# Kernel tuning notes

Measured on AMD Instinct MI355X. Metric: run time of the kernel, lower is better.

The kernel has to match this reference:

```python
import jax, jax.numpy as jnp
import numpy as np

DIM = 64; N_C = 2000; N_P = 1500; N_ATOMS = 40; L_PROT = 512
N_FP = 10000; N_WORD = 8000; DIM_D = 1024; DIM_P = 1024
L_GNN = 3; L_CNN = 3; L_GCN = 2; WIN = 5; B = 4096


def setup_inputs() -> dict:
    key = jax.random.key(0)
    ks = jax.random.split(key, 32)
    g = lambda i, shape, s=0.05: jax.random.normal(ks[i], shape, dtype=jnp.float32) * s
    inp = {}
    inp["idx_c"] = jax.random.randint(ks[0], (B,), 0, N_C)
    inp["idx_p"] = jax.random.randint(ks[1], (B,), 0, N_P)
    inp["compounds"] = jax.random.randint(ks[2], (N_C, N_ATOMS), 0, N_FP)
    inp["proteins"] = jax.random.randint(ks[3], (N_P, L_PROT), 0, N_WORD)
    a = (jax.random.uniform(ks[4], (N_C, N_ATOMS, N_ATOMS)) < 0.1).astype(jnp.float32)
    inp["adjacencies"] = jnp.clip(a + jnp.swapaxes(a, 1, 2) + jnp.eye(N_ATOMS), 0.0, 1.0)
    ac = (jax.random.uniform(ks[5], (N_C, N_C)) < 0.005).astype(jnp.float32)
    inp["A_c"] = jnp.clip(ac + ac.T + jnp.eye(N_C), 0.0, 1.0) / 20.0
    ap = (jax.random.uniform(ks[6], (N_P, N_P)) < 0.005).astype(jnp.float32)
    inp["A_p"] = jnp.clip(ap + ap.T + jnp.eye(N_P), 0.0, 1.0) / 20.0
    inp["embed_fp"] = g(7, (N_FP, DIM), 1.0)
    inp["embed_word"] = g(8, (N_WORD, DIM), 1.0)
    inp["Xs_c"] = g(9, (N_C, DIM), 1.0)
    inp["Xs_p"] = g(10, (N_P, DIM), 1.0)
    inp["drug_feat"] = g(11, (N_C, DIM_D), 1.0)
    inp["protein_feat"] = g(12, (N_P, DIM_P), 1.0)
    inp["W_gnn"] = g(13, (L_GNN, DIM, DIM)); inp["b_gnn"] = jnp.zeros((L_GNN, DIM), jnp.float32)
    inp["K_cnn"] = g(14, (L_CNN, 2 * WIN + 1, 2 * WIN + 1)); inp["b_cnn"] = jnp.zeros((L_CNN,), jnp.float32)
    inp["W_gcn_d"] = g(15, (L_GCN, DIM, DIM)); inp["b_gcn_d"] = jnp.zeros((L_GCN, DIM), jnp.float32)
    inp["W_gcn_p"] = g(16, (L_GCN, DIM, DIM)); inp["b_gcn_p"] = jnp.zeros((L_GCN, DIM), jnp.float32)
    inp["Wd1"] = g(17, (DIM_D, 2 * DIM)); inp["bd1"] = jnp.zeros((2 * DIM,), jnp.float32)
    inp["Wd2"] = g(18, (2 * DIM, DIM)); inp["bd2"] = jnp.zeros((DIM,), jnp.float32)
    inp["Wd3"] = g(19, (DIM, DIM)); inp["bd3"] = jnp.zeros((DIM,), jnp.float32)
    inp["Wp1"] = g(20, (DIM_P, 2 * DIM)); inp["bp1"] = jnp.zeros((2 * DIM,), jnp.float32)
    inp["Wp2"] = g(21, (2 * DIM, DIM)); inp["bp2"] = jnp.zeros((DIM,), jnp.float32)
    inp["Wp3"] = g(22, (DIM, DIM)); inp["bp3"] = jnp.zeros((DIM,), jnp.float32)
    inp["Wo1"] = g(23, (6 * DIM, 4 * DIM)); inp["bo1"] = jnp.zeros((4 * DIM,), jnp.float32)
    inp["Wo2"] = g(24, (4 * DIM, 4 * DIM)); inp["bo2"] = jnp.zeros((4 * DIM,), jnp.float32)
    inp["Wo3"] = g(25, (4 * DIM, 4 * DIM)); inp["bo3"] = jnp.zeros((4 * DIM,), jnp.float32)
    inp["W_int"] = g(26, (4 * DIM, 2)); inp["b_int"] = jnp.zeros((2,), jnp.float32)
    return inp


def reference(idx_c, idx_p, compounds, proteins, adjacencies, A_c, A_p,
              embed_fp, embed_word, Xs_c, Xs_p, drug_feat, protein_feat,
              W_gnn, b_gnn, K_cnn, b_cnn, W_gcn_d, b_gcn_d, W_gcn_p, b_gcn_p,
              Wd1, bd1, Wd2, bd2, Wd3, bd3, Wp1, bp1, Wp2, bp2, Wp3, bp3,
              Wo1, bo1, Wo2, bo2, Wo3, bo3, W_int, b_int):
    # ---- intrinsic compound embedding: batched GNN over all compounds.
    # (travInvolve's BFS selects a superset of idx_c; computing all rows is
    #  output-equivalent since only Xs_c_int[idx_c] is consumed.)
    xs = embed_fp[compounds]                                  # [N_c, A, d]
    for i in range(L_GNN):
        hs = jax.nn.relu(jnp.einsum('nad,de->nae', xs, W_gnn[i]) + b_gnn[i])
        xs = xs + jnp.einsum('nab,nbd->nad', adjacencies, hs)
    comp_int = jnp.mean(xs, axis=1)                           # [N_c, d]

    # ---- intrinsic protein embedding: batched single-channel 2D CNN (SAME pad)
    x = embed_word[proteins][:, None]                         # [N_p, 1, L, d]
    for i in range(L_CNN):
        x = jax.nn.relu(jax.lax.conv_general_dilated(
            x, K_cnn[i][None, None], (1, 1), [(WIN, WIN), (WIN, WIN)]) + b_cnn[i])
    prot_int = jnp.mean(x[:, 0], axis=1)                      # mean over length -> [N_p, d]

    # ---- relational GCN diffusion over global adjacency
    Xc = Xs_c
    for i in range(L_GCN):
        Xc = jax.nn.relu((A_c @ Xc) @ W_gcn_d[i] + b_gcn_d[i])
    Xp = Xs_p
    for i in range(L_GCN):
        Xp = jax.nn.relu((A_p @ Xp) @ W_gcn_p[i] + b_gcn_p[i])

    # ---- annotation MLPs
    fd = jax.nn.relu(drug_feat[idx_c] @ Wd1 + bd1)
    fd = jax.nn.relu(fd @ Wd2 + bd2)
    fd = jax.nn.relu(fd @ Wd3 + bd3)
    fp = jax.nn.relu(protein_feat[idx_p] @ Wp1 + bp1)
    fp = jax.nn.relu(fp @ Wp2 + bp2)
    fp = jax.nn.relu(fp @ Wp3 + bp3)

    cat = jnp.concatenate([comp_int[idx_c], Xc[idx_c], fd,
                           prot_int[idx_p], Xp[idx_p], fp], axis=1)  # [B, 6d]
    h = jax.nn.relu(cat @ Wo1 + bo1)
    h = jax.nn.relu(h @ Wo2 + bo2)
    h = jax.nn.relu(h @ Wo3 + bo3)
    return jax.nn.sigmoid(h @ W_int + b_int)                  # [B, 2]
```

## Files before the change

### kernel.cpp

```cpp
#include <hip/hip_runtime.h>
#include <math.h>

#define NC 2000
#define NP 1500
#define NA 40
#define LP 512
#define BSZ 4096
#define NW 8000
#define KPC 2048
#define KPP 1536

typedef _Float16 half8_t __attribute__((ext_vector_type(8)));
typedef _Float16 half4_t __attribute__((ext_vector_type(4)));
typedef float f32x4 __attribute__((ext_vector_type(4)));

__device__ __forceinline__ int swz_off(int row, int half_col)
{
    int b = half_col >> 3;
    return row * 128 + (((b & 8) | ((b ^ row) & 7)) << 3) + (half_col & 7);
}

__global__ void prep_all(
    const float* __restrict__ K_cnn, _Float16* __restrict__ wtab,
    const float* __restrict__ ew, _Float16* __restrict__ ehp,
    const float* __restrict__ df, const float* __restrict__ pf,
    const float* __restrict__ wd1, const float* __restrict__ wd2, const float* __restrict__ wd3,
    const float* __restrict__ wp1, const float* __restrict__ wp2, const float* __restrict__ wp3,
    const float* __restrict__ wo1, const float* __restrict__ wo2, const float* __restrict__ wo3,
    _Float16* __restrict__ dfh, _Float16* __restrict__ pfh,
    _Float16* __restrict__ wd1t, _Float16* __restrict__ wd2t, _Float16* __restrict__ wd3t,
    _Float16* __restrict__ wp1t, _Float16* __restrict__ wp2t, _Float16* __restrict__ wp3t,
    _Float16* __restrict__ wo1t, _Float16* __restrict__ wo2t, _Float16* __restrict__ wo3t,
    const float* __restrict__ Ac, const float* __restrict__ Ap,
    const float* __restrict__ Xc, const float* __restrict__ Xp,
    _Float16* __restrict__ Ahc, _Float16* __restrict__ Ahp,
    _Float16* __restrict__ Xtc, _Float16* __restrict__ Xtp,
    _Float16* __restrict__ Xtca, _Float16* __restrict__ Xtpa)
{
    int j = blockIdx.x * 256 + threadIdx.x;
    if (j < 16896) {
        int L = j / 5632, rem = j % 5632;
        int dr = rem >> 9, r2 = rem & 511, ln = r2 >> 3, i = r2 & 7;
        int dc = 8 * (ln >> 4) + i - (ln & 15);
        float v = (dc >= 0 && dc < 11) ? K_cnn[L * 121 + dr * 11 + dc] : 0.f;
        wtab[j] = (_Float16)v;
        return;
    }
    j -= 16896;
    if (j < NW * 80) {
        int w = j / 80, h = j - w * 80;
        float v = (h >= 13 && h < 77) ? ew[w * 64 + (h - 13)] : 0.f;
        ehp[j] = (_Float16)v;
        return;
    }
    j -= NW * 80;
    if (j < 2048000) { dfh[j] = (_Float16)df[j]; return; }
    j -= 2048000;
    if (j < 1536000) { pfh[j] = (_Float16)pf[j]; return; }
    j -= 1536000;
    if (j < 131072) { int n = j >> 10, k = j & 1023; wd1t[j] = (_Float16)wd1[k * 128 + n]; return; }
    j -= 131072;
    if (j < 8192)  { int n = j >> 7, k = j & 127; wd2t[j] = (_Float16)wd2[k * 64 + n]; return; }
    j -= 8192;
    if (j < 4096)  { int n = j >> 6, k = j & 63; wd3t[j] = (_Float16)wd3[k * 64 + n]; return; }
    j -= 4096;
    if (j < 131072) { int n = j >> 10, k = j & 1023; wp1t[j] = (_Float16)wp1[k * 128 + n]; return; }
    j -= 131072;
    if (j < 8192)  { int n = j >> 7, k = j & 127; wp2t[j] = (_Float16)wp2[k * 64 + n]; return; }
    j -= 8192;
    if (j < 4096)  { int n = j >> 6, k = j & 63; wp3t[j] = (_Float16)wp3[k * 64 + n]; return; }
    j -= 4096;
    if (j < 98304) { int n = j / 384, k = j - n * 384; wo1t[j] = (_Float16)wo1[k * 256 + n]; return; }
    j -= 98304;
    if (j < 65536) { int n = j >> 8, k = j & 255; wo2t[j] = (_Float16)wo2[k * 256 + n]; return; }
    j -= 65536;
    if (j < 65536) { int n = j >> 8, k = j & 255; wo3t[j] = (_Float16)wo3[k * 256 + n]; return; }
    j -= 65536;
    if (j < KPC * KPC) {
        int r = j >> 11, c = j & (KPC - 1);
        Ahc[j] = (_Float16)((r < NC && c < NC) ? Ac[(size_t)r * NC + c] : 0.f);
        return;
    }
    j -= KPC * KPC;
    if (j < KPP * KPP) {
        int r = j / KPP, c = j - r * KPP;
        Ahp[j] = (_Float16)((r < NP && c < NP) ? Ap[(size_t)r * NP + c] : 0.f);
        return;
    }
    j -= KPP * KPP;
    if (j < 64 * KPC) {
        int c = j >> 11, r = j & (KPC - 1);
        Xtc[j] = (_Float16)((r < NC) ? Xc[(size_t)r * 64 + c] : 0.f);
        return;
    }
    j -= 64 * KPC;
    if (j < 64 * KPP) {
        int c = j / KPP, r = j - c * KPP;
        Xtp[j] = (_Float16)((r < NP) ? Xp[(size_t)r * 64 + c] : 0.f);
        return;
    }
    j -= 64 * KPP;
    if (j < 64 * KPC) { Xtca[j] = (_Float16)0.f; return; }
    j -= 64 * KPC;
    if (j < 64 * KPP) { Xtpa[j] = (_Float16)0.f; }
}
#define PREP_TOTAL (16896 + NW * 80 + 2048000 + 1536000 + 131072 + 8192 + 4096 + 131072 + 8192 + 4096 + 98304 + 65536 + 65536 + KPC * KPC + KPP * KPP + 64 * KPC + 64 * KPP + 64 * KPC + 64 * KPP)

__global__ __launch_bounds__(256) void mega_kernel(
    const int* __restrict__ proteins, const _Float16* __restrict__ ehp,
    const half8_t* __restrict__ wtab, const float* __restrict__ b_cnn,
    float* __restrict__ prot_part,
    const int* __restrict__ compounds, const float* __restrict__ adjacencies,
    const float* __restrict__ embed_fp, const float* __restrict__ W_gnn,
    const float* __restrict__ b_gnn, _Float16* __restrict__ comp_h)
{
    __shared__ union SM {
        struct { half8_t bufA8[62 * 16]; half8_t bufB8[62 * 16]; } c;
        struct { float xs[40][68]; _Float16 hs[40][72];
                 _Float16 Ws[64][64]; _Float16 adjS[40][40]; float bS[64]; } g;
    } sm;
    const int bx = blockIdx.x;
    const int tid = threadIdx.x;

    if (bx < NC) {
        auto& G = sm.g;
        const int n = bx;
        for (int j = tid; j < 40 * 64; j += 256) {
            int r = j >> 6, c = j & 63;
            G.xs[r][c] = embed_fp[(size_t)compounds[n * NA + r] * 64 + c];
        }
        for (int j = tid; j < 1600; j += 256)
            G.adjS[j / 40][j % 40] = (_Float16)adjacencies[(size_t)n * 1600 + j];

        const int a0 = tid >> 3, cb = (tid & 7) * 8;
        const bool hasB = tid < 64;
        const int a1 = hasB ? (32 + (tid >> 3)) : 0;

        for (int l = 0; l < 3; ++l) {
            __syncthreads();
            for (int j = tid; j < 4096; j += 256) G.Ws[j >> 6][j & 63] = (_Float16)W_gnn[l * 4096 + j];
            if (tid < 64) G.bS[tid] = b_gnn[l * 64 + tid];
            __syncthreads();
            float accA[8], accB[8];
            #pragma unroll
            for (int j = 0; j < 8; ++j) { accA[j] = G.bS[cb + j]; accB[j] = accA[j]; }
            for (int d = 0; d < 64; ++d) {
                float xA = G.xs[a0][d];
                float xB = hasB ? G.xs[a1][d] : 0.f;
                #pragma unroll
                for (int j = 0; j < 8; ++j) {
                    float w = (float)G.Ws[d][cb + j];
                    accA[j] += xA * w;
                    accB[j] += xB * w;
                }
            }
            #pragma unroll
            for (int j = 0; j < 8; ++j) {
                G.hs[a0][cb + j] = (_Float16)fmaxf(accA[j], 0.f);
                if (hasB) G.hs[a1][cb + j] = (_Float16)fmaxf(accB[j], 0.f);
            }
            __syncthreads();
            float xA[8], xB[8];
            #pragma unroll
            for (int j = 0; j < 8; ++j) { xA[j] = G.xs[a0][cb + j]; xB[j] = hasB ? G.xs[a1][cb + j] : 0.f; }
            for (int b = 0; b < NA; ++b) {
                float adA = (float)G.adjS[a0][b];
                float adB = (float)G.adjS[a1][b];
                #pragma unroll
                for (int j = 0; j < 8; ++j) {
                    float h = (float)G.hs[b][cb + j];
                    xA[j] += adA * h;
                    xB[j] += adB * h;
                }
            }
            #pragma unroll
            for (int j = 0; j < 8; ++j) {
                G.xs[a0][cb + j] = xA[j];
                if (hasB) G.xs[a1][cb + j] = xB[j];
            }
        }
        __syncthreads();
        if (tid < 64) {
            float s = 0.f;
            for (int r = 0; r < NA; ++r) s += G.xs[r][tid];
            comp_h[n * 64 + tid] = (_Float16)(s * (1.0f / 40.0f));
        }
        return;
    }

    _Float16* bufA = (_Float16*)sm.c.bufA8;
    _Float16* bufB = (_Float16*)sm.c.bufB8;
    half8_t* bufA8 = sm.c.bufA8;
    half8_t* bufB8 = sm.c.bufB8;

    const int cb_ = bx - NC;
    const int tile = cb_ & 15, p = cb_ >> 4;
    const int t0 = tile * 32;
    const int lane = tid & 63, wid = tid >> 6;
    const int c0 = wid * 16;
    const int m = lane & 15, g = lane >> 4;

    half8_t z = {};
    for (int e = tid; e < 62 * 9; e += 256) {
        int i = e / 9, a = 1 + (e - 9 * i);
        int gr = t0 - 15 + i;
        half8_t v = z;
        if (gr >= 0 && gr < LP)
            v = *(const half8_t*)&ehp[(size_t)proteins[p * LP + gr] * 80 + 8 * a];
        *(half8_t*)&bufA[i * 128 + (((a & 8) | ((a ^ i) & 7)) << 3)] = v;
    }
    for (int e = tid; e < 62 * 4; e += 256) {
        int i = e >> 2, w = e & 3;
        if (w == 0)      bufA8[i * 16 + (8 | ((10 ^ i) & 7))] = z;
        else if (w == 1) bufB8[i * 16 + ((1 ^ i) & 7)] = z;
        else {
            int blk = 7 + w;
            bufB8[i * 16 + ((blk & 8) | ((blk ^ i) & 7))] = z;
        }
    }

    half8_t wf[11];
    auto load_wf = [&](int L) {
        #pragma unroll
        for (int dr = 0; dr < 11; ++dr) wf[dr] = wtab[L * 11 * 64 + dr * 64 + lane];
    };
    auto conv_tile = [&](const _Float16* src, int r0, float bias) -> f32x4 {
        f32x4 acc = {bias, bias, bias, bias};
        const int B0 = (c0 + 8) >> 3;
        #pragma unroll
        for (int dr = 0; dr < 11; ++dr) {
            int R = r0 - 5 + dr + m;
            int b = B0 + g;
            half8_t a = *(const half8_t*)&src[R * 128 + (((b & 8) | ((b ^ R) & 7)) << 3)];
            acc = __builtin_amdgcn_mfma_f32_16x16x32_f16(a, wf[dr], acc, 0, 0, 0);
        }
        return acc;
    };
    auto store_tile = [&](_Float16* dst, int r0, f32x4 acc) {
        int pc = c0 + 13 + m;
        #pragma unroll
        for (int j = 0; j < 4; ++j) {
            int row = r0 + 4 * g + j;
            int og = t0 - 15 + row;
            float v = fmaxf(acc[j], 0.f);
            dst[swz_off(row, pc)] = (_Float16)((og >= 0 && og < LP) ? v : 0.f);
        }
    };

    load_wf(0);
    __syncthreads();
    {
        float b0 = b_cnn[0];
        const int r0s[4] = {5, 21, 37, 41};
        #pragma unroll
        for (int k = 0; k < 4; ++k) store_tile(bufB, r0s[k], conv_tile(bufA, r0s[k], b0));
    }
    __syncthreads();
    load_wf(1);
    {
        float b1 = b_cnn[1];
        const int r0s[3] = {10, 26, 36};
        #pragma unroll
        for (int k = 0; k < 3; ++k) store_tile(bufA, r0s[k], conv_tile(bufB, r0s[k], b1));
    }
    __syncthreads();
    load_wf(2);
    {
        float b2 = b_cnn[2];
        float cs = 0.f;
        const int r0s[2] = {15, 31};
        #pragma unroll
        for (int k = 0; k < 2; ++k) {
            f32x4 acc = conv_tile(bufA, r0s[k], b2);
            #pragma unroll
            for (int j = 0; j < 4; ++j) cs += fmaxf(acc[j], 0.f);
        }
        cs += __shfl_xor(cs, 16, 64);
        cs += __shfl_xor(cs, 32, 64);
        if (lane < 16)
            prot_part[((size_t)p * 16 + tile) * 64 + c0 + lane] = cs;
    }
}

__global__ void cnn_reduce(const float* __restrict__ prot_part, _Float16* __restrict__ prot_h)
{
    const int p = blockIdx.x, c = threadIdx.x;
    float s = 0.f;
    for (int t = 0; t < 16; ++t) s += prot_part[((size_t)p * 16 + t) * 64 + c];
    prot_h[p * 64 + c] = (_Float16)(s * (1.0f / 512.0f));
}

__global__ __launch_bounds__(256) void spk_mfma_dual(
    const _Float16* __restrict__ Ah0, const _Float16* __restrict__ Xt0, float* __restrict__ P0, int M0, int Kp0,
    const _Float16* __restrict__ Ah1, const _Float16* __restrict__ Xt1, float* __restrict__ P1, int M1, int Kp1,
    int nx1)
{
    const _Float16* Ah; const _Float16* Xt; float* part; int M, Kp;
    if (blockIdx.z == 0) { Ah = Ah0; Xt = Xt0; part = P0; M = M0; Kp = Kp0; }
    else { if ((int)blockIdx.x >= nx1) return; Ah = Ah1; Xt = Xt1; part = P1; M = M1; Kp = Kp1; }

    const int tid = threadIdx.x, wid = tid >> 6, lane = tid & 63;
    const int m = lane & 15, g = lane >> 4;
    const int row0 = blockIdx.x * 64 + wid * 16;
    const int chunk = Kp >> 3, k0 = blockIdx.y * chunk;
    const _Float16* Apr = Ah + (size_t)(row0 + m) * Kp + 8 * g;
    f32x4 acc[4] = {};
    for (int kb = k0; kb < k0 + chunk; kb += 32) {
        half8_t af = *(const half8_t*)&Apr[kb];
        #pragma unroll
        for (int t = 0; t < 4; ++t) {
            half8_t bf = *(const half8_t*)&Xt[(size_t)(t * 16 + m) * Kp + kb + 8 * g];
            acc[t] = __builtin_amdgcn_mfma_f32_16x16x32_f16(af, bf, acc[t], 0, 0, 0);
        }
    }
    const int s = blockIdx.y;
    #pragma unroll
    for (int t = 0; t < 4; ++t)
        #pragma unroll
        for (int j = 0; j < 4; ++j) {
            int row = row0 + 4 * g + j;
            if (row < M) part[((size_t)s * M + row) * 64 + t * 16 + m] = acc[t][j];
        }
}

__global__ __launch_bounds__(256) void gcn_epi_dual(
    const float* __restrict__ P0, int M0, const float* __restrict__ W0, const float* __restrict__ b0,
    _Float16* __restrict__ H0, _Float16* __restrict__ XtN0, int Kp0,
    const float* __restrict__ P1, int M1, const float* __restrict__ W1, const float* __restrict__ b1,
    _Float16* __restrict__ H1, _Float16* __restrict__ XtN1, int Kp1, int nx1)
{
    const float* part; const float* W; const float* bias; _Float16* H; _Float16* XtN; int M, Kp;
    if (blockIdx.z == 0) { part = P0; W = W0; bias = b0; H = H0; XtN = XtN0; M = M0; Kp = Kp0; }
    else { if ((int)blockIdx.x >= nx1) return; part = P1; W = W1; bias = b1; H = H1; XtN = XtN1; M = M1; Kp = Kp1; }

    __shared__ float Ys[64][68];
    __shared__ float Ws[64][64];
    const int rb = blockIdx.x * 64;
    const int tid = threadIdx.x;
    for (int j = tid; j < 4096; j += 256) Ws[j >> 6][j & 63] = W[j];
    for (int j = tid; j < 4096; j += 256) {
        int r = j >> 6, c = j & 63;
        float sum = 0.f;
        if (rb + r < M)
            for (int t = 0; t < 8; ++t) sum += part[((size_t)t * M + rb + r) * 64 + c];
        Ys[r][c] = sum;
    }
    __syncthreads();
    const int tx = tid & 15, ty = tid >> 4;
    float acc[4][4];
    #pragma unroll
    for (int i = 0; i < 4; ++i)
        #pragma unroll
        for (int j = 0; j < 4; ++j) acc[i][j] = bias[tx * 4 + j];
    for (int d = 0; d < 64; ++d) {
        float a0 = Ys[ty * 4 + 0][d], a1 = Ys[ty * 4 + 1][d];
        float a2 = Ys[ty * 4 + 2][d], a3 = Ys[ty * 4 + 3][d];
        float4 w4 = *(const float4*)&Ws[d][tx * 4];
        acc[0][0] += a0 * w4.x; acc[0][1] += a0 * w4.y; acc[0][2] += a0 * w4.z; acc[0][3] += a0 * w4.w;
        acc[1][0] += a1 * w4.x; acc[1][1] += a1 * w4.y; acc[1][2] += a1 * w4.z; acc[1][3] += a1 * w4.w;
        acc[2][0] += a2 * w4.x; acc[2][1] += a2 * w4.y; acc[2][2] += a2 * w4.z; acc[2][3] += a2 * w4.w;
        acc[3][0] += a3 * w4.x; acc[3][1] += a3 * w4.y; acc[3][2] += a3 * w4.z; acc[3][3] += a3 * w4.w;
    }
    #pragma unroll
    for (int i = 0; i < 4; ++i) {
        int row = rb + ty * 4 + i;
        if (row < M) {
            #pragma unroll
            for (int j = 0; j < 4; ++j) {
                int col = tx * 4 + j;
                float v = fmaxf(acc[i][j], 0.f);
                if (H)   H[(size_t)row * 64 + col] = (_Float16)v;
                if (XtN) XtN[(size_t)col * Kp + row] = (_Float16)v;
            }
        }
    }
}

template<int NT, bool GATHER>
__global__ __launch_bounds__(256) void mfma_mlp(
    const _Float16* __restrict__ A0, const int* __restrict__ idx0,
    const _Float16* __restrict__ Bt0, const float* __restrict__ bias0, _Float16* __restrict__ C0,
    const _Float16* __restrict__ A1, const int* __restrict__ idx1,
    const _Float16* __restrict__ Bt1, const float* __restrict__ bias1, _Float16* __restrict__ C1,
    int K, int N)
{
    const _Float16* A; const int* idx; const _Float16* Bt; const float* bias; _Float16* C;
    if (blockIdx.z == 0) { A = A0; idx = idx0; Bt = Bt0; bias = bias0; C = C0; }
    else                 { A = A1; idx = idx1; Bt = Bt1; bias = bias1; C = C1; }
    const int tid = threadIdx.x, wid = tid >> 6, lane = tid & 63;
    const int m = lane & 15, g = lane >> 4;
    const int row0 = blockIdx.x * 64 + wid * 16;
    const int col0 = blockIdx.y * (NT * 16);
    size_t arow = GATHER ? (size_t)idx[row0 + m] : (size_t)(row0 + m);
    const _Float16* Ap = A + arow * (size_t)K + 8 * g;
    f32x4 acc[NT] = {};
    for (int kb = 0; kb < K; kb += 32) {
        half8_t af = *(const half8_t*)&Ap[kb];
        #pragma unroll
        for (int t = 0; t < NT; ++t) {
            half8_t bf = *(const half8_t*)&Bt[(size_t)(col0 + t * 16 + m) * K + kb + 8 * g];
            acc[t] = __builtin_amdgcn_mfma_f32_16x16x32_f16(af, bf, acc[t], 0, 0, 0);
        }
    }
    __shared__ float cb[4][16][17];
    const int rr = lane >> 2, c4 = (lane & 3) * 4;
    #pragma unroll
    for (int t = 0; t < NT; ++t) {
        #pragma unroll
        for (int j = 0; j < 4; ++j) cb[wid][4 * g + j][m] = acc[t][j];
        half4_t h;
        #pragma unroll
        for (int j = 0; j < 4; ++j)
            h[j] = (_Float16)fmaxf(cb[wid][rr][c4 + j] + bias[col0 + t * 16 + c4 + j], 0.f);
        *(half4_t*)&C[(size_t)(row0 + rr) * N + col0 + t * 16 + c4] = h;
    }
}

__global__ __launch_bounds__(256) void mfma_head1(
    const int* __restrict__ idx_c, const int* __restrict__ idx_p,
    const _Float16* __restrict__ ci, const _Float16* __restrict__ xc, const _Float16* __restrict__ fd,
    const _Float16* __restrict__ pi, const _Float16* __restrict__ xp, const _Float16* __restrict__ fp,
    const _Float16* __restrict__ Bt, const float* __restrict__ bias, _Float16* __restrict__ C)
{
    const int tid = threadIdx.x, wid = tid >> 6, lane = tid & 63;
    const int m = lane & 15, g = lane >> 4;
    const int row0 = blockIdx.x * 64 + wid * 16;
    const int col0 = blockIdx.y * 32;
    int ic = idx_c[row0 + m], ip = idx_p[row0 + m];
    const _Float16* segs[6] = {
        ci + (size_t)ic * 64 + 8 * g,  xc + (size_t)ic * 64 + 8 * g,
        fd + (size_t)(row0 + m) * 64 + 8 * g,
        pi + (size_t)ip * 64 + 8 * g,  xp + (size_t)ip * 64 + 8 * g,
        fp + (size_t)(row0 + m) * 64 + 8 * g };
    f32x4 acc[2] = {};
    #pragma unroll
    for (int kb = 0; kb < 384; kb += 32) {
        half8_t af = *(const half8_t*)&segs[kb / 64][kb & 63];
        #pragma unroll
        for (int t = 0; t < 2; ++t) {
            half8_t bf = *(const half8_t*)&Bt[(size_t)(col0 + t * 16 + m) * 384 + kb + 8 * g];
            acc[t] = __builtin_amdgcn_mfma_f32_16x16x32_f16(af, bf, acc[t], 0, 0, 0);
        }
    }
    __shared__ float cb[4][16][17];
    const int rr = lane >> 2, c4 = (lane & 3) * 4;
    #pragma unroll
    for (int t = 0; t < 2; ++t) {
        #pragma unroll
        for (int j = 0; j < 4; ++j) cb[wid][4 * g + j][m] = acc[t][j];
        half4_t h;
        #pragma unroll
        for (int j = 0; j < 4; ++j)
            h[j] = (_Float16)fmaxf(cb[wid][rr][c4 + j] + bias[col0 + t * 16 + c4 + j], 0.f);
        *(half4_t*)&C[(size_t)(row0 + rr) * 256 + col0 + t * 16 + c4] = h;
    }
}

__global__ __launch_bounds__(256) void mfma_head3(
    const _Float16* __restrict__ A, const _Float16* __restrict__ Bt,
    const float* __restrict__ bias, const float* __restrict__ Wi, const float* __restrict__ bi,
    float* __restrict__ out)
{
    const int tid = threadIdx.x, wid = tid >> 6, lane = tid & 63;
    const int m = lane & 15, g = lane >> 4;
    const int row0 = blockIdx.x * 64 + wid * 16;
    const _Float16* Ap = A + (size_t)(row0 + m) * 256 + 8 * g;
    f32x4 acc[16] = {};
    for (int kb = 0; kb < 256; kb += 32) {
        half8_t af = *(const half8_t*)&Ap[kb];
        #pragma unroll
        for (int t = 0; t < 16; ++t) {
            half8_t bf = *(const half8_t*)&Bt[(size_t)(t * 16 + m) * 256 + kb + 8 * g];
            acc[t] = __builtin_amdgcn_mfma_f32_16x16x32_f16(af, bf, acc[t], 0, 0, 0);
        }
    }
    float p0[4] = {}, p1[4] = {};
    #pragma unroll
    for (int t = 0; t < 16; ++t) {
        float w0 = Wi[(t * 16 + m) * 2], w1 = Wi[(t * 16 + m) * 2 + 1];
        float bc = bias[t * 16 + m];
        #pragma unroll
        for (int j = 0; j < 4; ++j) {
            float v = fmaxf(acc[t][j] + bc, 0.f);
            p0[j] += v * w0; p1[j] += v * w1;
        }
    }
    #pragma unroll
    for (int d = 1; d < 16; d <<= 1) {
        #pragma unroll
        for (int j = 0; j < 4; ++j) {
            p0[j] += __shfl_xor(p0[j], d, 64);
            p1[j] += __shfl_xor(p1[j], d, 64);
        }
    }
    if (m == 0) {
        float B0 = bi[0], B1 = bi[1];
        #pragma unroll
        for (int j = 0; j < 4; ++j) {
            int r = row0 + 4 * g + j;
            out[r * 2 + 0] = 1.f / (1.f + expf(-(p0[j] + B0)));
            out[r * 2 + 1] = 1.f / (1.f + expf(-(p1[j] + B1)));
        }
    }
}

extern "C" void kernel_launch(void* const* d_in, const int* in_sizes, int n_in,
                              void* d_out, int out_size, void* d_ws, size_t ws_size,
                              hipStream_t stream)
{
    const int*   idx_c        = (const int*)  d_in[0];
    const int*   idx_p        = (const int*)  d_in[1];
    const int*   compounds    = (const int*)  d_in[2];
    const int*   proteins     = (const int*)  d_in[3];
    const float* adjacencies  = (const float*)d_in[4];
    const float* A_c          = (const float*)d_in[5];
    const float* A_p          = (const float*)d_in[6];
    const float* embed_fp     = (const float*)d_in[7];
    const float* embed_word   = (const float*)d_in[8];
    const float* Xs_c         = (const float*)d_in[9];
    const float* Xs_p         = (const float*)d_in[10];
    const float* drug_feat    = (const float*)d_in[11];
    const float* protein_feat = (const float*)d_in[12];
    const float* W_gnn        = (const float*)d_in[13];
    const float* b_gnn        = (const float*)d_in[14];
    const float* K_cnn        = (const float*)d_in[15];
    const float* b_cnn        = (const float*)d_in[16];
    const float* W_gcn_d      = (const float*)d_in[17];
    const float* b_gcn_d      = (const float*)d_in[18];
    const float* W_gcn_p      = (const float*)d_in[19];
    const float* b_gcn_p      = (const float*)d_in[20];
    const float* Wd1 = (const float*)d_in[21]; const float* bd1 = (const float*)d_in[22];
    const float* Wd2 = (const float*)d_in[23]; const float* bd2 = (const float*)d_in[24];
    const float* Wd3 = (const float*)d_in[25]; const float* bd3 = (const float*)d_in[26];
    const float* Wp1 = (const float*)d_in[27]; const float* bp1 = (const float*)d_in[28];
    const float* Wp2 = (const float*)d_in[29]; const float* bp2 = (const float*)d_in[30];
    const float* Wp3 = (const float*)d_in[31]; const float* bp3 = (const float*)d_in[32];
    const float* Wo1 = (const float*)d_in[33]; const float* bo1 = (const float*)d_in[34];
    const float* Wo2 = (const float*)d_in[35]; const float* bo2 = (const float*)d_in[36];
    const float* Wo3 = (const float*)d_in[37]; const float* bo3 = (const float*)d_in[38];
    const float* W_int = (const float*)d_in[39]; const float* b_int = (const float*)d_in[40];

    float* ws = (float*)d_ws;
    float* prot_part = ws; ws += NP * 16 * 64;
    float* wtab_g    = ws; ws += 8448;
    float* ehp_g     = ws; ws += NW * 40;
    float* part_c    = ws; ws += 8 * NC * 64;
    float* part_p    = ws; ws += 8 * NP * 64;
    _Float16* Ah_c  = (_Float16*)ws; ws += KPC * KPC / 2;
    _Float16* Ah_p  = (_Float16*)ws; ws += KPP * KPP / 2;
    _Float16* Xt_c  = (_Float16*)ws; ws += 32 * KPC;
    _Float16* Xt_p  = (_Float16*)ws; ws += 32 * KPP;
    _Float16* Xt_ca = (_Float16*)ws; ws += 32 * KPC;
    _Float16* Xt_pa = (_Float16*)ws; ws += 32 * KPP;
    _Float16* comp_h  = (_Float16*)ws; ws += NC * 32;
    _Float16* prot_h  = (_Float16*)ws; ws += NP * 32;
    _Float16* Xcb_h   = (_Float16*)ws; ws += NC * 32;
    _Float16* Xpb_h   = (_Float16*)ws; ws += NP * 32;
    _Float16* drug_h  = (_Float16*)ws; ws += NC * 512;
    _Float16* protf_h = (_Float16*)ws; ws += NP * 512;
    _Float16* wd1t = (_Float16*)ws; ws += 65536;
    _Float16* wd2t = (_Float16*)ws; ws += 4096;
    _Float16* wd3t = (_Float16*)ws; ws += 2048;
    _Float16* wp1t = (_Float16*)ws; ws += 65536;
    _Float16* wp2t = (_Float16*)ws; ws += 4096;
    _Float16* wp3t = (_Float16*)ws; ws += 2048;
    _Float16* wo1t = (_Float16*)ws; ws += 49152;
    _Float16* wo2t = (_Float16*)ws; ws += 32768;
    _Float16* wo3t = (_Float16*)ws; ws += 32768;
    _Float16* fd1h = (_Float16*)ws; ws += BSZ * 64;
    _Float16* fd2h = (_Float16*)ws; ws += BSZ * 32;
    _Float16* fd3h = (_Float16*)ws; ws += BSZ * 32;
    _Float16* fp1h = (_Float16*)ws; ws += BSZ * 64;
    _Float16* fp2h = (_Float16*)ws; ws += BSZ * 32;
    _Float16* fp3h = (_Float16*)ws; ws += BSZ * 32;
    _Float16* h1h  = (_Float16*)ws; ws += BSZ * 128;
    _Float16* h2h  = (_Float16*)ws; ws += BSZ * 128;
    (void)ws_size; (void)in_sizes; (void)n_in; (void)out_size;

    prep_all<<<(PREP_TOTAL + 255) / 256, 256, 0, stream>>>(
        K_cnn, (_Float16*)wtab_g, embed_word, (_Float16*)ehp_g,
        drug_feat, protein_feat, Wd1, Wd2, Wd3, Wp1, Wp2, Wp3, Wo1, Wo2, Wo3,
        drug_h, protf_h, wd1t, wd2t, wd3t, wp1t, wp2t, wp3t, wo1t, wo2t, wo3t,
        A_c, A_p, Xs_c, Xs_p, Ah_c, Ah_p, Xt_c, Xt_p, Xt_ca, Xt_pa);
    mega_kernel<<<NC + 16 * NP, 256, 0, stream>>>(
        proteins, (const _Float16*)ehp_g, (const half8_t*)wtab_g, b_cnn, prot_part,
        compounds, adjacencies, embed_fp, W_gnn, b_gnn, comp_h);
    cnn_reduce<<<NP, 64, 0, stream>>>(prot_part, prot_h);
    spk_mfma_dual<<<dim3(32, 8, 2), 256, 0, stream>>>(
        Ah_c, Xt_c, part_c, NC, KPC, Ah_p, Xt_p, part_p, NP, KPP, 24);
    gcn_epi_dual<<<dim3(32, 1, 2), 256, 0, stream>>>(
        part_c, NC, W_gcn_d, b_gcn_d, nullptr, Xt_ca, KPC,
        part_p, NP, W_gcn_p, b_gcn_p, nullptr, Xt_pa, KPP, 24);
    spk_mfma_dual<<<dim3(32, 8, 2), 256, 0, stream>>>(
        Ah_c, Xt_ca, part_c, NC, KPC, Ah_p, Xt_pa, part_p, NP, KPP, 24);
    gcn_epi_dual<<<dim3(32, 1, 2), 256, 0, stream>>>(
        part_c, NC, W_gcn_d + 4096, b_gcn_d + 64, Xcb_h, nullptr, KPC,
        part_p, NP, W_gcn_p + 4096, b_gcn_p + 64, Xpb_h, nullptr, KPP, 24);
    mfma_mlp<2, true ><<<dim3(64, 4, 2), 256, 0, stream>>>(
        drug_h, idx_c, wd1t, bd1, fd1h, protf_h, idx_p, wp1t, bp1, fp1h, 1024, 128);
    mfma_mlp<1, false><<<dim3(64, 4, 2), 256, 0, stream>>>(
        fd1h, nullptr, wd2t, bd2, fd2h, fp1h, nullptr, wp2t, bp2, fp2h, 128, 64);
    mfma_mlp<1, false><<<dim3(64, 4, 2), 256, 0, stream>>>(
        fd2h, nullptr, wd3t, bd3, fd3h, fp2h, nullptr, wp3t, bp3, fp3h, 64, 64);
    mfma_head1<<<dim3(64, 8), 256, 0, stream>>>(idx_c, idx_p, comp_h, Xcb_h, fd3h,
                                                prot_h, Xpb_h, fp3h, wo1t, bo1, h1h);
    mfma_mlp<2, false><<<dim3(64, 8, 1), 256, 0, stream>>>(
        h1h, nullptr, wo2t, bo2, h2h, h1h, nullptr, wo2t, bo2, h2h, 256, 256);
    mfma_head3<<<64, 256, 0, stream>>>(h2h, wo3t, bo3, W_int, b_int, (float*)d_out);
}
```

Baseline: 424.2 us.

## Rewrite compound GNN layers with MFMA using pre-transposed fp16 weights

The per-compound GNN in the mega kernel moves from scalar FMA loops over shared memory to 16x16x32 fp16 MFMA instructions for both the weight projection and the adjacency aggregation. The GNN weights are transposed and converted to fp16 once in the prep kernel, and the adjacency fragments are kept in registers. The node state is now held in fp16 instead of fp32 between layers, which cuts shared-memory traffic and per-layer weight staging but lowers the precision of the residual accumulation. Atom rows are padded from 40 to 48 to fit 16-row tiles.

Measured after the change: 349.0 us. 17.7% less time.

```diff
diff --git a/kernel.cpp b/kernel.cpp
--- a/kernel.cpp
+++ b/kernel.cpp
@@ -31,6 +31,7 @@
     _Float16* __restrict__ wd1t, _Float16* __restrict__ wd2t, _Float16* __restrict__ wd3t,
     _Float16* __restrict__ wp1t, _Float16* __restrict__ wp2t, _Float16* __restrict__ wp3t,
     _Float16* __restrict__ wo1t, _Float16* __restrict__ wo2t, _Float16* __restrict__ wo3t,
+    const float* __restrict__ wgnn, _Float16* __restrict__ wgt,
     const float* __restrict__ Ac, const float* __restrict__ Ap,
     const float* __restrict__ Xc, const float* __restrict__ Xp,
     _Float16* __restrict__ Ahc, _Float16* __restrict__ Ahp,
@@ -76,6 +77,9 @@
     j -= 65536;
     if (j < 65536) { int n = j >> 8, k = j & 255; wo3t[j] = (_Float16)wo3[k * 256 + n]; return; }
     j -= 65536;
+    if (j < 12288) { int l = j >> 12, rem = j & 4095, nn = rem >> 6, k = rem & 63;
+                     wgt[j] = (_Float16)wgnn[l * 4096 + k * 64 + nn]; return; }
+    j -= 12288;
     if (j < KPC * KPC) {
         int r = j >> 11, c = j & (KPC - 1);
         Ahc[j] = (_Float16)((r < NC && c < NC) ? Ac[(size_t)r * NC + c] : 0.f);
@@ -104,85 +108,91 @@
     j -= 64 * KPC;
     if (j < 64 * KPP) { Xtpa[j] = (_Float16)0.f; }
 }
-#define PREP_TOTAL (16896 + NW * 80 + 2048000 + 1536000 + 131072 + 8192 + 4096 + 131072 + 8192 + 4096 + 98304 + 65536 + 65536 + KPC * KPC + KPP * KPP + 64 * KPC + 64 * KPP + 64 * KPC + 64 * KPP)
+#define PREP_TOTAL (16896 + NW * 80 + 2048000 + 1536000 + 131072 + 8192 + 4096 + 131072 + 8192 + 4096 + 98304 + 65536 + 65536 + 12288 + KPC * KPC + KPP * KPP + 64 * KPC + 64 * KPP + 64 * KPC + 64 * KPP)
 
 __global__ __launch_bounds__(256) void mega_kernel(
     const int* __restrict__ proteins, const _Float16* __restrict__ ehp,
     const half8_t* __restrict__ wtab, const float* __restrict__ b_cnn,
     float* __restrict__ prot_part,
     const int* __restrict__ compounds, const float* __restrict__ adjacencies,
-    const float* __restrict__ embed_fp, const float* __restrict__ W_gnn,
+    const float* __restrict__ embed_fp, const _Float16* __restrict__ wgt,
     const float* __restrict__ b_gnn, _Float16* __restrict__ comp_h)
 {
     __shared__ union SM {
         struct { half8_t bufA8[62 * 16]; half8_t bufB8[62 * 16]; } c;
-        struct { float xs[40][68]; _Float16 hs[40][72];
-                 _Float16 Ws[64][64]; _Float16 adjS[40][40]; float bS[64]; } g;
+        struct { _Float16 xs[48 * 72]; _Float16 hsT[64 * 72]; } g;
     } sm;
     const int bx = blockIdx.x;
     const int tid = threadIdx.x;
+    const int lane = tid & 63, wid = tid >> 6;
+    const int m = lane & 15, g = lane >> 4;
 
     if (bx < NC) {
         auto& G = sm.g;
         const int n = bx;
-        for (int j = tid; j < 40 * 64; j += 256) {
+        const int colL = wid * 16 + m;
+
+        for (int j = tid; j < 48 * 64; j += 256) {
             int r = j >> 6, c = j & 63;
-            G.xs[r][c] = embed_fp[(size_t)compounds[n * NA + r] * 64 + c];
-        }
-        for (int j = tid; j < 1600; j += 256)
-            G.adjS[j / 40][j % 40] = (_Float16)adjacencies[(size_t)n * 1600 + j];
-
-        const int a0 = tid >> 3, cb = (tid & 7) * 8;
-        const bool hasB = tid < 64;
-        const int a1 = hasB ? (32 + (tid >> 3)) : 0;
+            _Float16 v = (_Float16)0.f;
+            if (r < 40) v = (_Float16)embed_fp[(size_t)compounds[n * NA + r] * 64 + c];
+            G.xs[r * 72 + c] = v;
+        }
+        for (int j = tid; j < 64 * 72 / 8; j += 256) ((half8_t*)G.hsT)[j] = (half8_t){};
+
+        half8_t adjf[3][2];
+        #pragma unroll
+        for (int t = 0; t < 3; ++t)
+            #pragma unroll
+            for (int s = 0; s < 2; ++s) {
+                half8_t v = {};
+                int row = t * 16 + m, k0 = s * 32 + 8 * g;
+                if (row < 40 && k0 < 40) {
+                    const float* src = &adjacencies[(size_t)n * 1600 + row * 40 + k0];
+                    #pragma unroll
+                    for (int i = 0; i < 8; ++i) v[i] = (_Float16)src[i];
+                }
+                adjf[t][s] = v;
+            }
+        __syncthreads();
 
         for (int l = 0; l < 3; ++l) {
-            __syncthreads();
-            for (int j = tid; j < 4096; j += 256) G.Ws[j >> 6][j & 63] = (_Float16)W_gnn[l * 4096 + j];
-            if (tid < 64) G.bS[tid] = b_gnn[l * 64 + tid];
-            __syncthreads();
-            float accA[8], accB[8];
+            float bcol = b_gnn[l * 64 + colL];
             #pragma unroll
-            for (int j = 0; j < 8; ++j) { accA[j] = G.bS[cb + j]; accB[j] = accA[j]; }
-            for (int d = 0; d < 64; ++d) {
-                float xA = G.xs[a0][d];
-                float xB = hasB ? G.xs[a1][d] : 0.f;
+            for (int t = 0; t < 3; ++t) {
+                f32x4 acc = {bcol, bcol, bcol, bcol};
                 #pragma unroll
-                for (int j = 0; j < 8; ++j) {
-                    float w = (float)G.Ws[d][cb + j];
-                    accA[j] += xA * w;
-                    accB[j] += xB * w;
+                for (int s = 0; s < 2; ++s) {
+                    half8_t a = *(const half8_t*)&G.xs[(t * 16 + m) * 72 + s * 32 + 8 * g];
+                    half8_t b = *(const half8_t*)&wgt[(size_t)(l * 64 + colL) * 64 + s * 32 + 8 * g];
+                    acc = __builtin_amdgcn_mfma_f32_16x16x32_f16(a, b, acc, 0, 0, 0);
                 }
-            }
-            #pragma unroll
-            for (int j = 0; j < 8; ++j) {
-                G.hs[a0][cb + j] = (_Float16)fmaxf(accA[j], 0.f);
-                if (hasB) G.hs[a1][cb + j] = (_Float16)fmaxf(accB[j], 0.f);
+                half4_t h4;
+                #pragma unroll
+                for (int j = 0; j < 4; ++j) h4[j] = (_Float16)fmaxf(acc[j], 0.f);
+                *(half4_t*)&G.hsT[colL * 72 + t * 16 + 4 * g] = h4;
             }
             __syncthreads();
-            float xA[8], xB[8];
             #pragma unroll
-            for (int j = 0; j < 8; ++j) { xA[j] = G.xs[a0][cb + j]; xB[j] = hasB ? G.xs[a1][cb + j] : 0.f; }
-            for (int b = 0; b < NA; ++b) {
-                float adA = (float)G.adjS[a0][b];
-                float adB = (float)G.adjS[a1][b];
+            for (int t = 0; t < 3; ++t) {
+                f32x4 acc;
                 #pragma unroll
-                for (int j = 0; j < 8; ++j) {
-                    float h = (float)G.hs[b][cb + j];
-                    xA[j] += adA * h;
-                    xB[j] += adB * h;
+                for (int j = 0; j < 4; ++j)
+                    acc[j] = (float)G.xs[(t * 16 + 4 * g + j) * 72 + colL];
+                #pragma unroll
+                for (int s = 0; s < 2; ++s) {
+                    half8_t b = *(const half8_t*)&G.hsT[colL * 72 + s * 32 + 8 * g];
+                    acc = __builtin_amdgcn_mfma_f32_16x16x32_f16(adjf[t][s], b, acc, 0, 0, 0);
                 }
+                #pragma unroll
+                for (int j = 0; j < 4; ++j)
+                    G.xs[(t * 16 + 4 * g + j) * 72 + colL] = (_Float16)acc[j];
             }
-            #pragma unroll
-            for (int j = 0; j < 8; ++j) {
-                G.xs[a0][cb + j] = xA[j];
-                if (hasB) G.xs[a1][cb + j] = xB[j];
-            }
-        }
-        __syncthreads();
+            __syncthreads();
+        }
         if (tid < 64) {
             float s = 0.f;
-            for (int r = 0; r < NA; ++r) s += G.xs[r][tid];
+            for (int r = 0; r < 40; ++r) s += (float)G.xs[r * 72 + tid];
             comp_h[n * 64 + tid] = (_Float16)(s * (1.0f / 40.0f));
         }
         return;
@@ -196,9 +206,7 @@
     const int cb_ = bx - NC;
     const int tile = cb_ & 15, p = cb_ >> 4;
     const int t0 = tile * 32;
-    const int lane = tid & 63, wid = tid >> 6;
     const int c0 = wid * 16;
-    const int m = lane & 15, g = lane >> 4;
 
     half8_t z = {};
     for (int e = tid; e < 62 * 9; e += 256) {
@@ -552,6 +560,7 @@
     _Float16* Xt_p  = (_Float16*)ws; ws += 32 * KPP;
     _Float16* Xt_ca = (_Float16*)ws; ws += 32 * KPC;
     _Float16* Xt_pa = (_Float16*)ws; ws += 32 * KPP;
+    _Float16* wgt_g = (_Float16*)ws; ws += 6144;
     _Float16* comp_h  = (_Float16*)ws; ws += NC * 32;
     _Float16* prot_h  = (_Float16*)ws; ws += NP * 32;
     _Float16* Xcb_h   = (_Float16*)ws; ws += NC * 32;
@@ -581,10 +590,11 @@
         K_cnn, (_Float16*)wtab_g, embed_word, (_Float16*)ehp_g,
         drug_feat, protein_feat, Wd1, Wd2, Wd3, Wp1, Wp2, Wp3, Wo1, Wo2, Wo3,
         drug_h, protf_h, wd1t, wd2t, wd3t, wp1t, wp2t, wp3t, wo1t, wo2t, wo3t,
+        W_gnn, wgt_g,
         A_c, A_p, Xs_c, Xs_p, Ah_c, Ah_p, Xt_c, Xt_p, Xt_ca, Xt_pa);
     mega_kernel<<<NC + 16 * NP, 256, 0, stream>>>(
         proteins, (const _Float16*)ehp_g, (const half8_t*)wtab_g, b_cnn, prot_part,
-        compounds, adjacencies, embed_fp, W_gnn, b_gnn, comp_h);
+        compounds, adjacencies, embed_fp, wgt_g, b_gnn, comp_h);
     cnn_reduce<<<NP, 64, 0, stream>>>(prot_part, prot_h);
     spk_mfma_dual<<<dim3(32, 8, 2), 256, 0, stream>>>(
         Ah_c, Xt_c, part_c, NC, KPC, Ah_p, Xt_p, part_p, NP, KPP, 24);
```
